# Performance work log

Hardware: AMD Instinct MI355X
Metric: run time of the kernel (lower is better)

Reference implementation:

```python
import jax, jax.numpy as jnp
import numpy as np

DIM = 1024
HEADS = 16
HEAD_DIM = DIM // HEADS


def setup_inputs() -> dict:
    key = jax.random.key(0)
    ks = jax.random.split(key, 12)
    B, Tq, Tk = 2, 2048, 2048
    inp = {
        "query": jax.random.normal(ks[0], (B, Tq, DIM), jnp.float32),
        "key": jax.random.normal(ks[1], (B, Tk, DIM), jnp.float32),
        "value": jax.random.normal(ks[2], (B, Tk, DIM), jnp.float32),
        "mask": jax.random.randint(ks[3], (B, 1, Tq, Tk), 0, 2, jnp.int32),
        # xavier-uniform projection weights (stored [out,in] like torch), zero biases
        "wq": jax.random.uniform(ks[4], (DIM, DIM), jnp.float32, -1.0, 1.0) * np.sqrt(6.0 / (2 * DIM)),
        "wk": jax.random.uniform(ks[5], (DIM, DIM), jnp.float32, -1.0, 1.0) * np.sqrt(6.0 / (2 * DIM)),
        "wv": jax.random.uniform(ks[6], (DIM, DIM), jnp.float32, -1.0, 1.0) * np.sqrt(6.0 / (2 * DIM)),
        "wo": jax.random.uniform(ks[7], (DIM, DIM), jnp.float32, -1.0, 1.0) * np.sqrt(6.0 / (2 * DIM)),
        "bq": jnp.zeros((DIM,), jnp.float32),
        "bk": jnp.zeros((DIM,), jnp.float32),
        "bv": jnp.zeros((DIM,), jnp.float32),
        "bo": jnp.zeros((DIM,), jnp.float32),
    }
    return inp


def reference(query, key, value, mask, wq, wk, wv, wo, bq, bk, bv, bo):
    B, Tq, C = query.shape
    Tk = key.shape[1]
    scale = 1.0 / np.sqrt(HEAD_DIM)
    # projections (torch Linear: x @ W.T + b) -> [B, H, T, Dh]
    q = (query @ wq.T + bq).reshape(B, Tq, HEADS, HEAD_DIM).transpose(0, 2, 1, 3)
    k = (key @ wk.T + bk).reshape(B, Tk, HEADS, HEAD_DIM).transpose(0, 2, 1, 3)
    v = (value @ wv.T + bv).reshape(B, Tk, HEADS, HEAD_DIM).transpose(0, 2, 1, 3)
    scores = jnp.einsum("bhqd,bhkd->bhqk", q, k) * scale
    scores = jnp.clip(scores, -100.0, 100.0)
    scores = jnp.where(mask == 0, -jnp.inf, scores)
    attn = jax.nn.softmax(scores, axis=-1)  # dropout is identity in eval
    out = jnp.einsum("bhqk,bhkd->bhqd", attn, v)
    out = out.transpose(0, 2, 1, 3).reshape(B, Tq, HEADS * HEAD_DIM)
    return out @ wo.T + bo
```

## Files before the change

### kernel.cpp

```cpp
#include <hip/hip_runtime.h>
#include <hip/hip_bf16.h>
#include <stdint.h>


typedef __bf16 bf16;
typedef __bf16 bf16x4 __attribute__((ext_vector_type(4)));
typedef __bf16 bf16x8 __attribute__((ext_vector_type(8)));
typedef float f32x4 __attribute__((ext_vector_type(4)));
typedef short s16x4 __attribute__((ext_vector_type(4)));

#define MFMA_BF16(a, b, c) __builtin_amdgcn_mfma_f32_16x16x32_bf16((a), (b), (c), 0, 0, 0)

__device__ __forceinline__ f32x4 mfma16(bf16x4 a, bf16x4 b, f32x4 c) {
  return __builtin_amdgcn_mfma_f32_16x16x16bf16_1k(
      __builtin_bit_cast(s16x4, a), __builtin_bit_cast(s16x4, b), c, 0, 0, 0);
}

__device__ __forceinline__ void async_load16(const void* g, void* l) {
  __builtin_amdgcn_global_load_lds((const __attribute__((address_space(1))) void*)g,
                                   (__attribute__((address_space(3))) void*)l, 16, 0, 0);
}

__global__ __launch_bounds__(256) void cvt_f32_bf16(
    const float* __restrict__ s0, const float* __restrict__ s1, const float* __restrict__ s2,
    const float* __restrict__ s3, const float* __restrict__ s4, const float* __restrict__ s5,
    const float* __restrict__ s6,
    bf16* __restrict__ d0, bf16* __restrict__ d1, bf16* __restrict__ d2,
    bf16* __restrict__ d3, bf16* __restrict__ d4, bf16* __restrict__ d5,
    bf16* __restrict__ d6) {
  const int z = blockIdx.y;
  const float* s = (z == 0) ? s0 : (z == 1) ? s1 : (z == 2) ? s2 : (z == 3) ? s3
                   : (z == 4) ? s4 : (z == 5) ? s5 : s6;
  bf16* d = (z == 0) ? d0 : (z == 1) ? d1 : (z == 2) ? d2 : (z == 3) ? d3
            : (z == 4) ? d4 : (z == 5) ? d5 : d6;
  const int n4 = (z < 3) ? (4 * 1024 * 1024 / 4) : (1024 * 1024 / 4);
  const int stride = gridDim.x * 256;
  for (int i = blockIdx.x * 256 + threadIdx.x; i < n4; i += stride) {
    const float4 v = ((const float4*)s)[i];
    bf16x4 o;
    o[0] = (bf16)v.x; o[1] = (bf16)v.y; o[2] = (bf16)v.z; o[3] = (bf16)v.w;
    ((bf16x4*)d)[i] = o;
  }
}

__global__ __launch_bounds__(256) void pack_mask_kernel(const int* __restrict__ mask,
                                                        unsigned long long* __restrict__ bits) {
  const int t = blockIdx.x * 256 + threadIdx.x;
  const int v = mask[t];
  const unsigned long long b = __ballot(v != 0);
  if ((threadIdx.x & 63) == 0) bits[t >> 6] = b;
}

__global__ __launch_bounds__(256) void gemm_bt_bias(
    const bf16* __restrict__ X0, const bf16* __restrict__ X1, const bf16* __restrict__ X2,
    const bf16* __restrict__ W0, const bf16* __restrict__ W1, const bf16* __restrict__ W2,
    const float* __restrict__ Bi0, const float* __restrict__ Bi1, const float* __restrict__ Bi2,
    bf16* __restrict__ O0, bf16* __restrict__ O1, bf16* __restrict__ O2,
    float* __restrict__ OF, int K, int N, int vz, int f32out, float qs) {
  const int z = blockIdx.z;
  const bf16* X   = (z == 0) ? X0  : (z == 1) ? X1  : X2;
  const bf16* W   = (z == 0) ? W0  : (z == 1) ? W1  : W2;
  const float* Bi = (z == 0) ? Bi0 : (z == 1) ? Bi1 : Bi2;
  bf16* O         = (z == 0) ? O0  : (z == 1) ? O1  : O2;

  __shared__ __align__(16) unsigned char smem_raw[34816];
  bf16* As  = (bf16*)smem_raw;
  bf16* Bs  = As + 128 * 64;
  bf16* Tt  = (bf16*)smem_raw;
  float* Tf = (float*)smem_raw;

  const int tid = threadIdx.x;
  const int lane = tid & 63;
  const int w = tid >> 6;
  const int la = lane & 15;
  const int qa = lane >> 4;
  const int m0 = blockIdx.x * 128;
  const int n0 = blockIdx.y * 128;
  const int wm = (w & 1) * 64;
  const int wn = (w >> 1) * 64;

  f32x4 acc[4][4];
  for (int i = 0; i < 4; ++i)
    for (int j = 0; j < 4; ++j) acc[i][j] = (f32x4){0.f, 0.f, 0.f, 0.f};

  for (int k0 = 0; k0 < K; k0 += 64) {
    for (int i = 0; i < 4; ++i) {
      const int cb = i * 256 + w * 64;
      const int c = cb + lane;
      const int row = c >> 3;
      const int cc = (c & 7) * 8;
      async_load16(X + (size_t)(m0 + row) * K + k0 + cc, As + (size_t)cb * 8);
      async_load16(W + (size_t)(n0 + row) * K + k0 + cc, Bs + (size_t)cb * 8);
    }
    __syncthreads();
    for (int kk = 0; kk < 64; kk += 32) {
      bf16x8 af[4], bfr[4];
      for (int mt = 0; mt < 4; ++mt)
        af[mt] = *(const bf16x8*)&As[(wm + mt * 16 + la) * 64 + kk + qa * 8];
      for (int nt = 0; nt < 4; ++nt)
        bfr[nt] = *(const bf16x8*)&Bs[(wn + nt * 16 + la) * 64 + kk + qa * 8];
      for (int mt = 0; mt < 4; ++mt)
        for (int nt = 0; nt < 4; ++nt)
          acc[mt][nt] = MFMA_BF16(af[mt], bfr[nt], acc[mt][nt]);
    }
    __syncthreads();
  }

  if (f32out) {
    for (int pass = 0; pass < 2; ++pass) {
      if ((w & 1) == pass) {
        for (int mt = 0; mt < 4; ++mt)
          for (int nt = 0; nt < 4; ++nt)
            for (int r = 0; r < 4; ++r) {
              const int rl = mt * 16 + qa * 4 + r;
              const int cl = wn + nt * 16 + la;
              Tf[rl * 132 + cl] = acc[mt][nt][r] + Bi[n0 + cl];
            }
      }
      __syncthreads();
      for (int i = 0; i < 8; ++i) {
        const int rl = i * 8 + (tid >> 5);
        const int cl = (tid & 31) * 4;
        const float4 vv = *(const float4*)&Tf[rl * 132 + cl];
        *(float4*)&OF[(size_t)(m0 + pass * 64 + rl) * N + n0 + cl] = vv;
      }
      __syncthreads();
    }
  } else if (z != vz) {
    const float sc = (z == 0) ? qs : 1.0f;
    for (int mt = 0; mt < 4; ++mt)
      for (int nt = 0; nt < 4; ++nt)
        for (int r = 0; r < 4; ++r) {
          const int rl = wm + mt * 16 + qa * 4 + r;
          const int cl = wn + nt * 16 + la;
          Tt[rl * 136 + cl] = (bf16)((acc[mt][nt][r] + Bi[n0 + cl]) * sc);
        }
    __syncthreads();
    for (int i = 0; i < 8; ++i) {
      const int rl = i * 16 + (tid >> 4);
      const int cc = (tid & 15) * 8;
      *(bf16x8*)&O[(size_t)(m0 + rl) * N + n0 + cc] = *(const bf16x8*)&Tt[rl * 136 + cc];
    }
  } else {
    for (int mt = 0; mt < 4; ++mt)
      for (int nt = 0; nt < 4; ++nt)
        for (int r = 0; r < 4; ++r) {
          const int rl = wm + mt * 16 + qa * 4 + r;
          const int cl = wn + nt * 16 + la;
          Tt[cl * 136 + rl] = (bf16)(acc[mt][nt][r] + Bi[n0 + cl]);
        }
    __syncthreads();
    const int bb = m0 >> 11;
    const int kt0 = (m0 & 2047) >> 6;
    const int h0 = n0 >> 6;
    for (int i = 0; i < 8; ++i) {
      const int gi = i * 256 + tid;
      const int c = gi & 511;
      const int ktb = (gi >> 9) & 1;
      const int hb = gi >> 10;
      const int dt2 = (c >> 8) & 1;
      const int ntc = (c >> 6) & 3;
      const int tq = (c >> 3) & 7;
      const int qac = tq & 3;
      const int lac = ((tq >> 2) << 3) + (c & 7);
      const int clA = hb * 64 + dt2 * 32 + lac;
      const int rlb = ktb * 64 + ntc * 16 + qac * 4;
      const bf16x4 lo4 = *(const bf16x4*)&Tt[clA * 136 + rlb];
      const bf16x4 hi4 = *(const bf16x4*)&Tt[(clA + 16) * 136 + rlb];
      bf16x8 outc;
      for (int j = 0; j < 4; ++j) { outc[j] = lo4[j]; outc[j + 4] = hi4[j]; }
      const size_t g16 = ((size_t)((bb * 16 + h0 + hb) * 32) + kt0 + ktb) * 512 + c;
      *(bf16x8*)&O[g16 * 8] = outc;
    }
  }
}

__global__ __launch_bounds__(256, 3) void attn_kernel(
    const bf16* __restrict__ Qp, const bf16* __restrict__ Kp, const bf16* __restrict__ Vt,
    const unsigned long long* __restrict__ mbits, bf16* __restrict__ AO) {
  __shared__ bf16 Kb[2][64 * 64];
  __shared__ bf16 Vb[2][64 * 64];

  const int tid = threadIdx.x;
  const int lane = tid & 63;
  const int w = tid >> 6;
  const int la = lane & 15;
  const int qa = lane >> 4;
  const int la7 = la & 7;
  const int b = blockIdx.y >> 4;
  const int h = blockIdx.y & 15;
  const int q0 = blockIdx.x * 64 + w * 16;

  const size_t kbase = (size_t)(b * 2048) * 1024 + h * 64;
  const unsigned long long* mrow = mbits + ((size_t)(b * 2048 + q0 + la)) * 32;

  const int cb0 = w * 64;
  const int cb1 = 256 + w * 64;
  const int c0 = cb0 + lane, c1 = cb1 + lane;
  const int r0 = c0 >> 3, j0 = (c0 & 7) ^ (r0 & 7);
  const int r1 = c1 >> 3, j1 = (c1 & 7) ^ (r1 & 7);
  const bf16* kp0 = Kp + kbase + (size_t)r0 * 1024 + j0 * 8;
  const bf16* kp1 = Kp + kbase + (size_t)r1 * 1024 + j1 * 8;
  const size_t vbase16 = (size_t)((b * 16 + h) * 32) * 512;
  const bf16* vp0 = Vt + (vbase16 + c0) * 8;
  const bf16* vp1 = Vt + (vbase16 + c1) * 8;

  bf16x8 qf[2];
  for (int kk = 0; kk < 2; ++kk)
    qf[kk] = *(const bf16x8*)&Qp[(size_t)(b * 2048 + q0 + la) * 1024 + h * 64 + kk * 32 + qa * 8];

  bf16x4 ones4;
  for (int j = 0; j < 4; ++j) ones4[j] = (bf16)1.0f;

  const int vsig = (la & 7) + 8 * (qa + 4 * (la >> 3));

  f32x4 oacc[5];
  for (int d = 0; d < 5; ++d) oacc[d] = (f32x4){0.f, 0.f, 0.f, 0.f};

  async_load16(kp0, &Kb[0][cb0 * 8]);
  async_load16(kp1, &Kb[0][cb1 * 8]);
  async_load16(vp0, &Vb[0][cb0 * 8]);
  async_load16(vp1, &Vb[0][cb1 * 8]);
  unsigned long long mv = mrow[0];
  __syncthreads();

  for (int kt = 0; kt < 32; ++kt) {
    const int p = kt & 1;
    const bf16* Kc = Kb[p];
    const bf16* Vc = Vb[p];

    unsigned long long mvn = 0;
    if (kt < 31) {
      bf16* Kn = Kb[p ^ 1];
      bf16* Vn = Vb[p ^ 1];
      kp0 += 64 * 1024; kp1 += 64 * 1024;
      vp0 += 4096;      vp1 += 4096;
      async_load16(kp0, &Kn[cb0 * 8]);
      async_load16(kp1, &Kn[cb1 * 8]);
      async_load16(vp0, &Vn[cb0 * 8]);
      async_load16(vp1, &Vn[cb1 * 8]);
      mvn = mrow[kt + 1];
    }

    f32x4 s[4];
    for (int nt = 0; nt < 4; ++nt) s[nt] = (f32x4){0.f, 0.f, 0.f, 0.f};
#pragma unroll
    for (int kk = 0; kk < 2; ++kk)
#pragma unroll
      for (int nt = 0; nt < 4; ++nt) {
        const bf16x8 kf = *(const bf16x8*)&Kc[(nt * 16 + la) * 64 + (((kk * 4 + qa) ^ la7) * 8)];
        s[nt] = MFMA_BF16(kf, qf[kk], s[nt]);
      }

    bf16x8 vv[2][4];
#pragma unroll
    for (int dt2 = 0; dt2 < 2; ++dt2)
#pragma unroll
      for (int nt = 0; nt < 4; ++nt)
        vv[dt2][nt] = *(const bf16x8*)&Vc[((dt2 * 4 + nt) * 64 + vsig) * 8];

    const unsigned long long mvs = mv >> (qa * 4);
    const uint32_t mlo = (uint32_t)mvs, mhi = (uint32_t)(mvs >> 32);
    bf16x4 pfr[4];
#pragma unroll
    for (int nt = 0; nt < 4; ++nt) {
      const uint32_t mw = ((nt & 2) ? mhi : mlo) >> ((nt & 1) * 16);
#pragma unroll
      for (int r = 0; r < 4; ++r) {
        const float bitf = (float)((mw >> r) & 1u);
        pfr[nt][r] = (bf16)(bitf * exp2f(s[nt][r]));
      }
    }

#pragma unroll
    for (int nt = 0; nt < 4; ++nt) {
#pragma unroll
      for (int dt2 = 0; dt2 < 2; ++dt2) {
        const bf16x4 lo = __builtin_shufflevector(vv[dt2][nt], vv[dt2][nt], 0, 1, 2, 3);
        const bf16x4 hi = __builtin_shufflevector(vv[dt2][nt], vv[dt2][nt], 4, 5, 6, 7);
        oacc[2 * dt2]     = mfma16(lo, pfr[nt], oacc[2 * dt2]);
        oacc[2 * dt2 + 1] = mfma16(hi, pfr[nt], oacc[2 * dt2 + 1]);
      }
      oacc[4] = mfma16(ones4, pfr[nt], oacc[4]);
    }

    mv = mvn;
    __syncthreads();
  }

  const float rl = 1.0f / oacc[4][0];
  for (int dt = 0; dt < 4; ++dt) {
    bf16x4 o4;
    for (int r = 0; r < 4; ++r) o4[r] = (bf16)(oacc[dt][r] * rl);
    *(bf16x4*)&AO[(size_t)(b * 2048 + q0 + la) * 1024 + h * 64 + dt * 16 + qa * 4] = o4;
  }
}

extern "C" void kernel_launch(void* const* d_in, const int* in_sizes, int n_in,
                              void* d_out, int out_size, void* d_ws, size_t ws_size,
                              hipStream_t stream) {
  const float* q    = (const float*)d_in[0];
  const float* k    = (const float*)d_in[1];
  const float* v    = (const float*)d_in[2];
  const int*   mask = (const int*)d_in[3];
  const float* wq   = (const float*)d_in[4];
  const float* wk   = (const float*)d_in[5];
  const float* wv   = (const float*)d_in[6];
  const float* wo   = (const float*)d_in[7];
  const float* bq   = (const float*)d_in[8];
  const float* bk   = (const float*)d_in[9];
  const float* bv   = (const float*)d_in[10];
  const float* bo   = (const float*)d_in[11];

  const size_t M4 = (size_t)4 * 1024 * 1024, M1 = (size_t)1024 * 1024;
  bf16* qb  = (bf16*)d_ws;
  bf16* kb  = qb + M4;
  bf16* vb  = kb + M4;
  bf16* wqb = vb + M4;
  bf16* wkb = wqb + M1;
  bf16* wvb = wkb + M1;
  bf16* wob = wvb + M1;
  bf16* Qp  = wob + M1;
  bf16* Kp  = Qp + M4;
  bf16* Vt  = Kp + M4;
  unsigned long long* mb = (unsigned long long*)(Vt + M4);
  bf16* AO  = qb;
  float* out = (float*)d_out;

  const float QSCALE = 0.18033688011112042f;

  cvt_f32_bf16<<<dim3(2048, 7), dim3(256), 0, stream>>>(
      q, k, v, wq, wk, wv, wo, qb, kb, vb, wqb, wkb, wvb, wob);
  pack_mask_kernel<<<dim3(8388608 / 256), dim3(256), 0, stream>>>(mask, mb);
  gemm_bt_bias<<<dim3(32, 8, 3), dim3(256), 0, stream>>>(
      qb, kb, vb, wqb, wkb, wvb, bq, bk, bv, Qp, Kp, Vt, nullptr, 1024, 1024, 2, 0, QSCALE);
  attn_kernel<<<dim3(32, 32), dim3(256), 0, stream>>>(Qp, Kp, Vt, mb, AO);
  gemm_bt_bias<<<dim3(32, 8, 1), dim3(256), 0, stream>>>(
      AO, AO, AO, wob, wob, wob, bo, bo, bo, nullptr, nullptr, nullptr, out, 1024, 1024, -1, 1, 1.0f);
}
```

Baseline: 300.8 us.

## Process two 16-row query groups per wave in attention kernel

Each wave now computes two query row-groups against every loaded K/V tile. Each block therefore covers 128 queries and the grid is halved. This doubles reuse of shared-memory K/V fragments and halves global K/V traffic. In exchange it raises register use (launch bounds lowered to 2 blocks per CU) and leaves fewer blocks to fill the GPU.

```diff
diff --git a/kernel.cpp b/kernel.cpp
--- a/kernel.cpp
+++ b/kernel.cpp
@@ -175,7 +175,7 @@
   }
 }
 
-__global__ __launch_bounds__(256, 3) void attn_kernel(
+__global__ __launch_bounds__(256, 2) void attn_kernel(
     const bf16* __restrict__ Qp, const bf16* __restrict__ Kp, const bf16* __restrict__ Vt,
     const unsigned long long* __restrict__ mbits, bf16* __restrict__ AO) {
   __shared__ bf16 Kb[2][64 * 64];
@@ -189,10 +189,11 @@
   const int la7 = la & 7;
   const int b = blockIdx.y >> 4;
   const int h = blockIdx.y & 15;
-  const int q0 = blockIdx.x * 64 + w * 16;
+  const int q0 = blockIdx.x * 128 + w * 32;
 
   const size_t kbase = (size_t)(b * 2048) * 1024 + h * 64;
-  const unsigned long long* mrow = mbits + ((size_t)(b * 2048 + q0 + la)) * 32;
+  const unsigned long long* mrow0 = mbits + ((size_t)(b * 2048 + q0 + la)) * 32;
+  const unsigned long long* mrow1 = mrow0 + 16 * 32;
 
   const int cb0 = w * 64;
   const int cb1 = 256 + w * 64;
@@ -205,23 +206,27 @@
   const bf16* vp0 = Vt + (vbase16 + c0) * 8;
   const bf16* vp1 = Vt + (vbase16 + c1) * 8;
 
-  bf16x8 qf[2];
-  for (int kk = 0; kk < 2; ++kk)
-    qf[kk] = *(const bf16x8*)&Qp[(size_t)(b * 2048 + q0 + la) * 1024 + h * 64 + kk * 32 + qa * 8];
+  bf16x8 qf[2][2];
+  for (int g = 0; g < 2; ++g)
+    for (int kk = 0; kk < 2; ++kk)
+      qf[g][kk] = *(const bf16x8*)&Qp[(size_t)(b * 2048 + q0 + g * 16 + la) * 1024 +
+                                      h * 64 + kk * 32 + qa * 8];
 
   bf16x4 ones4;
   for (int j = 0; j < 4; ++j) ones4[j] = (bf16)1.0f;
 
   const int vsig = (la & 7) + 8 * (qa + 4 * (la >> 3));
 
-  f32x4 oacc[5];
-  for (int d = 0; d < 5; ++d) oacc[d] = (f32x4){0.f, 0.f, 0.f, 0.f};
+  f32x4 oacc[2][5];
+  for (int g = 0; g < 2; ++g)
+    for (int d = 0; d < 5; ++d) oacc[g][d] = (f32x4){0.f, 0.f, 0.f, 0.f};
 
   async_load16(kp0, &Kb[0][cb0 * 8]);
   async_load16(kp1, &Kb[0][cb1 * 8]);
   async_load16(vp0, &Vb[0][cb0 * 8]);
   async_load16(vp1, &Vb[0][cb1 * 8]);
-  unsigned long long mv = mrow[0];
+  unsigned long long mv0 = mrow0[0];
+  unsigned long long mv1 = mrow1[0];
   __syncthreads();
 
   for (int kt = 0; kt < 32; ++kt) {
@@ -229,7 +234,7 @@
     const bf16* Kc = Kb[p];
     const bf16* Vc = Vb[p];
 
-    unsigned long long mvn = 0;
+    unsigned long long mvn0 = 0, mvn1 = 0;
     if (kt < 31) {
       bf16* Kn = Kb[p ^ 1];
       bf16* Vn = Vb[p ^ 1];
@@ -239,17 +244,20 @@
       async_load16(kp1, &Kn[cb1 * 8]);
       async_load16(vp0, &Vn[cb0 * 8]);
       async_load16(vp1, &Vn[cb1 * 8]);
-      mvn = mrow[kt + 1];
-    }
-
-    f32x4 s[4];
-    for (int nt = 0; nt < 4; ++nt) s[nt] = (f32x4){0.f, 0.f, 0.f, 0.f};
+      mvn0 = mrow0[kt + 1];
+      mvn1 = mrow1[kt + 1];
+    }
+
+    f32x4 s[2][4];
+    for (int g = 0; g < 2; ++g)
+      for (int nt = 0; nt < 4; ++nt) s[g][nt] = (f32x4){0.f, 0.f, 0.f, 0.f};
 #pragma unroll
     for (int kk = 0; kk < 2; ++kk)
 #pragma unroll
       for (int nt = 0; nt < 4; ++nt) {
         const bf16x8 kf = *(const bf16x8*)&Kc[(nt * 16 + la) * 64 + (((kk * 4 + qa) ^ la7) * 8)];
-        s[nt] = MFMA_BF16(kf, qf[kk], s[nt]);
+        s[0][nt] = MFMA_BF16(kf, qf[0][kk], s[0][nt]);
+        s[1][nt] = MFMA_BF16(kf, qf[1][kk], s[1][nt]);
       }
 
     bf16x8 vv[2][4];
@@ -259,40 +267,46 @@
       for (int nt = 0; nt < 4; ++nt)
         vv[dt2][nt] = *(const bf16x8*)&Vc[((dt2 * 4 + nt) * 64 + vsig) * 8];
 
-    const unsigned long long mvs = mv >> (qa * 4);
-    const uint32_t mlo = (uint32_t)mvs, mhi = (uint32_t)(mvs >> 32);
-    bf16x4 pfr[4];
-#pragma unroll
-    for (int nt = 0; nt < 4; ++nt) {
-      const uint32_t mw = ((nt & 2) ? mhi : mlo) >> ((nt & 1) * 16);
-#pragma unroll
-      for (int r = 0; r < 4; ++r) {
-        const float bitf = (float)((mw >> r) & 1u);
-        pfr[nt][r] = (bf16)(bitf * exp2f(s[nt][r]));
-      }
-    }
-
-#pragma unroll
-    for (int nt = 0; nt < 4; ++nt) {
-#pragma unroll
-      for (int dt2 = 0; dt2 < 2; ++dt2) {
-        const bf16x4 lo = __builtin_shufflevector(vv[dt2][nt], vv[dt2][nt], 0, 1, 2, 3);
-        const bf16x4 hi = __builtin_shufflevector(vv[dt2][nt], vv[dt2][nt], 4, 5, 6, 7);
-        oacc[2 * dt2]     = mfma16(lo, pfr[nt], oacc[2 * dt2]);
-        oacc[2 * dt2 + 1] = mfma16(hi, pfr[nt], oacc[2 * dt2 + 1]);
-      }
-      oacc[4] = mfma16(ones4, pfr[nt], oacc[4]);
-    }
-
-    mv = mvn;
-    __syncthreads();
-  }
-
-  const float rl = 1.0f / oacc[4][0];
-  for (int dt = 0; dt < 4; ++dt) {
-    bf16x4 o4;
-    for (int r = 0; r < 4; ++r) o4[r] = (bf16)(oacc[dt][r] * rl);
-    *(bf16x4*)&AO[(size_t)(b * 2048 + q0 + la) * 1024 + h * 64 + dt * 16 + qa * 4] = o4;
+#pragma unroll
+    for (int g = 0; g < 2; ++g) {
+      const unsigned long long mvs = (g == 0 ? mv0 : mv1) >> (qa * 4);
+      const uint32_t mlo = (uint32_t)mvs, mhi = (uint32_t)(mvs >> 32);
+      bf16x4 pfr[4];
+#pragma unroll
+      for (int nt = 0; nt < 4; ++nt) {
+        const uint32_t mw = ((nt & 2) ? mhi : mlo) >> ((nt & 1) * 16);
+#pragma unroll
+        for (int r = 0; r < 4; ++r) {
+          const float bitf = (float)((mw >> r) & 1u);
+          pfr[nt][r] = (bf16)(bitf * exp2f(s[g][nt][r]));
+        }
+      }
+#pragma unroll
+      for (int nt = 0; nt < 4; ++nt) {
+#pragma unroll
+        for (int dt2 = 0; dt2 < 2; ++dt2) {
+          const bf16x4 lo = __builtin_shufflevector(vv[dt2][nt], vv[dt2][nt], 0, 1, 2, 3);
+          const bf16x4 hi = __builtin_shufflevector(vv[dt2][nt], vv[dt2][nt], 4, 5, 6, 7);
+          oacc[g][2 * dt2]     = mfma16(lo, pfr[nt], oacc[g][2 * dt2]);
+          oacc[g][2 * dt2 + 1] = mfma16(hi, pfr[nt], oacc[g][2 * dt2 + 1]);
+        }
+        oacc[g][4] = mfma16(ones4, pfr[nt], oacc[g][4]);
+      }
+    }
+
+    mv0 = mvn0;
+    mv1 = mvn1;
+    __syncthreads();
+  }
+
+#pragma unroll
+  for (int g = 0; g < 2; ++g) {
+    const float rl = 1.0f / oacc[g][4][0];
+    for (int dt = 0; dt < 4; ++dt) {
+      bf16x4 o4;
+      for (int r = 0; r < 4; ++r) o4[r] = (bf16)(oacc[g][dt][r] * rl);
+      *(bf16x4*)&AO[(size_t)(b * 2048 + q0 + g * 16 + la) * 1024 + h * 64 + dt * 16 + qa * 4] = o4;
+    }
   }
 }
 
@@ -334,7 +348,7 @@
   pack_mask_kernel<<<dim3(8388608 / 256), dim3(256), 0, stream>>>(mask, mb);
   gemm_bt_bias<<<dim3(32, 8, 3), dim3(256), 0, stream>>>(
       qb, kb, vb, wqb, wkb, wvb, bq, bk, bv, Qp, Kp, Vt, nullptr, 1024, 1024, 2, 0, QSCALE);
-  attn_kernel<<<dim3(32, 32), dim3(256), 0, stream>>>(Qp, Kp, Vt, mb, AO);
+  attn_kernel<<<dim3(16, 32), dim3(256), 0, stream>>>(Qp, Kp, Vt, mb, AO);
   gemm_bt_bias<<<dim3(32, 8, 1), dim3(256), 0, stream>>>(
       AO, AO, AO, wob, wob, wob, bo, bo, bo, nullptr, nullptr, nullptr, out, 1024, 1024, -1, 1, 1.0f);
 }
```

Result: no change. 303.9 us (+1.0%).
